# Performance work log

Hardware: AMD Instinct MI355X
Metric: run time of the kernel (lower is better)

Reference implementation:

```python
import jax, jax.numpy as jnp
import numpy as np

B, S, D = 2, 2048, 1024
H = 16  # num_content_vectors
HD = D // H


def setup_inputs() -> dict:
    key = jax.random.key(0)
    k1, k2, k3 = jax.random.split(key, 3)
    encoded = jax.random.normal(k1, (B, S, D), dtype=jnp.float32)
    # FusedDense(embed_dim, 2*embed_dim): weight [2D, D], bias [2D] (torch Linear layout)
    W = jax.random.normal(k2, (2 * D, D), dtype=jnp.float32) * (1.0 / np.sqrt(D))
    bias = jax.random.normal(k3, (2 * D,), dtype=jnp.float32) * 0.01
    return {"encoded": encoded, "W": W, "bias": bias}


def reference(encoded, W, bias):
    b, s, d = encoded.shape
    h = H
    hd = d // h
    # fused QK projection
    qk = jnp.einsum('bsd,ed->bse', encoded, W) + bias  # [b, s, 2d]
    qk = qk.reshape(b, s, 2, h, hd)
    q = qk[:, :, 0]  # [b, s, h, hd]
    k = qk[:, :, 1]
    scale = 1.0 / np.sqrt(hd)
    scores = jnp.einsum('bthd,bshd->bhts', q, k * scale)  # [b, h, s, s]
    causal_mask = jnp.triu(jnp.full((s, s), -10000.0, dtype=scores.dtype), 1)
    scores = scores + causal_mask
    return jax.nn.softmax(scores, axis=-1)
```

## Files before the change

### kernel.cpp

```cpp
#include <hip/hip_runtime.h>

#define S 2048
#define D 1024
#define H 16
#define HD 64

typedef _Float16 half8 __attribute__((ext_vector_type(8)));
typedef _Float16 half4v __attribute__((ext_vector_type(4)));
typedef float f32x4 __attribute__((ext_vector_type(4)));

__device__ __forceinline__ float fast_exp2(float x) {
#if __has_builtin(__builtin_amdgcn_exp2f)
    return __builtin_amdgcn_exp2f(x);
#else
    return exp2f(x);
#endif
}

__global__ __launch_bounds__(256) void cvt_f32_f16(const float* __restrict__ src,
                                                   _Float16* __restrict__ dst, int n4) {
    const int i = blockIdx.x * 256 + threadIdx.x;
    if (i >= n4) return;
    const float4 v = ((const float4*)src)[i];
    half4v h;
    h.x = (_Float16)v.x; h.y = (_Float16)v.y;
    h.z = (_Float16)v.z; h.w = (_Float16)v.w;
    ((half4v*)dst)[i] = h;
}

__global__ __launch_bounds__(256) void proj_mfma(const _Float16* __restrict__ Ah,
                                                 const _Float16* __restrict__ Wh,
                                                 const float* __restrict__ bias,
                                                 _Float16* __restrict__ qbuf,
                                                 _Float16* __restrict__ kbuf) {
    __shared__ __align__(16) _Float16 As[4][128][8];
    __shared__ __align__(16) _Float16 Bs[4][128][8];
    const int tid = threadIdx.x;
    const int w   = tid >> 6;
    const int l   = tid & 63;
    const int l15 = l & 15;
    const int l4  = l >> 4;
    const int wy  = w >> 1;
    const int wx  = w & 1;
    const int m0  = blockIdx.x * 128;
    const int n0  = blockIdx.y * 128;

    f32x4 acc[4][4] = {};

    for (int k0 = 0; k0 < D; k0 += 32) {
        if (k0) __syncthreads();
        #pragma unroll
        for (int p = 0; p < 2; ++p) {
            const int slot = p * 256 + tid;
            const int sub = slot >> 7, row = slot & 127;
            *(uint4*)&As[sub][row][0] = *(const uint4*)(Ah + (size_t)(m0 + row) * D + k0 + sub * 8);
            *(uint4*)&Bs[sub][row][0] = *(const uint4*)(Wh + (size_t)(n0 + row) * D + k0 + sub * 8);
        }
        __syncthreads();

        half8 af[4], bf[4];
        #pragma unroll
        for (int i = 0; i < 4; ++i)
            af[i] = *(const half8*)&As[l4][wy * 64 + i * 16 + l15][0];
        #pragma unroll
        for (int j = 0; j < 4; ++j)
            bf[j] = *(const half8*)&Bs[l4][wx * 64 + j * 16 + l15][0];
        #pragma unroll
        for (int i = 0; i < 4; ++i)
            #pragma unroll
            for (int j = 0; j < 4; ++j)
                acc[i][j] = __builtin_amdgcn_mfma_f32_16x16x32_f16(af[i], bf[j], acc[i][j], 0, 0, 0);
    }

    #pragma unroll
    for (int j = 0; j < 4; ++j) {
        const int e   = n0 + wx * 64 + j * 16 + l15;
        const bool isq = (e < D);
        const int eh  = isq ? e : (e - D);
        const int h   = eh >> 6;
        const int hd  = eh & 63;
        _Float16* dst = isq ? qbuf : kbuf;
        const float sc = isq ? 1.0f : 0.18033688f;
        const float bv = bias[e];
        #pragma unroll
        for (int i = 0; i < 4; ++i) {
            #pragma unroll
            for (int r = 0; r < 4; ++r) {
                const int m  = m0 + wy * 64 + i * 16 + l4 * 4 + r;
                const int bb = m >> 11;
                const int ss = m & (S - 1);
                dst[((size_t)(bb * H + h) * S + ss) * HD + hd] = (_Float16)((acc[i][j][r] + bv) * sc);
            }
        }
    }
}

__global__ __launch_bounds__(256) void attn_fused(const _Float16* __restrict__ qbuf,
                                                  const _Float16* __restrict__ kbuf,
                                                  float* __restrict__ out) {
    const int tid = threadIdx.x;
    const int w   = tid >> 6;
    const int l   = tid & 63;
    const int l15 = l & 15;
    const int l4  = l >> 4;

    const int bid  = blockIdx.x;
    const int xcd  = bid & 7;
    const int slot = bid >> 3;
    const int k    = slot >> 5;
    int tsr = slot & 31;
    if (k & 2) tsr = (tsr + 16) & 31;
    const int ts = (k & 1) ? (31 - tsr) : tsr;
    const int z  = xcd * 4 + k;
    const int t0 = ts * 64;

    const _Float16* Qg = qbuf + (size_t)z * S * HD;
    const _Float16* Kg = kbuf + (size_t)z * S * HD;
    float* outz = out + (size_t)z * S * S;

    const _Float16* qrow = Qg + (size_t)(t0 + w * 16 + l15) * HD + l4 * 8;
    const half8 qf0 = *(const half8*)qrow;
    const half8 qf1 = *(const half8*)(qrow + 32);

    const int nst  = ts + 1;
    const int trow = t0 + w * 16 + l4 * 4;
    const _Float16* kbase = Kg + (size_t)l15 * HD + l4 * 8;

    float sum_r[4] = {0.f, 0.f, 0.f, 0.f};

    for (int st = 0; st < nst; ++st) {
        const _Float16* kp = kbase + (size_t)st * (64 * HD);
        f32x4 c[4] = {};
        #pragma unroll
        for (int j = 0; j < 4; ++j) {
            const half8 kf0 = *(const half8*)(kp + j * (16 * HD));
            const half8 kf1 = *(const half8*)(kp + j * (16 * HD) + 32);
            c[j] = __builtin_amdgcn_mfma_f32_16x16x32_f16(qf0, kf0, c[j], 0, 0, 0);
            c[j] = __builtin_amdgcn_mfma_f32_16x16x32_f16(qf1, kf1, c[j], 0, 0, 0);
        }
        if (st == ts) {
            #pragma unroll
            for (int j = 0; j < 4; ++j) {
                const int scol = t0 + j * 16 + l15;
                #pragma unroll
                for (int r = 0; r < 4; ++r)
                    if (scol > trow + r) c[j][r] = -1e30f;
            }
        }
        #pragma unroll
        for (int j = 0; j < 4; ++j)
            #pragma unroll
            for (int r = 0; r < 4; ++r)
                sum_r[r] += fast_exp2(c[j][r]);
    }

    float inv_l[4];
    #pragma unroll
    for (int r = 0; r < 4; ++r) {
        float s = sum_r[r];
        s += __shfl_xor(s, 1, 16);
        s += __shfl_xor(s, 2, 16);
        s += __shfl_xor(s, 4, 16);
        s += __shfl_xor(s, 8, 16);
        inv_l[r] = 1.0f / s;
    }

    float* wrow = outz + (size_t)trow * S + l15;
    for (int st = 0; st < nst; ++st) {
        const int s0 = st * 64;
        const _Float16* kp = kbase + (size_t)st * (64 * HD);
        f32x4 c[4] = {};
        #pragma unroll
        for (int j = 0; j < 4; ++j) {
            const half8 kf0 = *(const half8*)(kp + j * (16 * HD));
            const half8 kf1 = *(const half8*)(kp + j * (16 * HD) + 32);
            c[j] = __builtin_amdgcn_mfma_f32_16x16x32_f16(qf0, kf0, c[j], 0, 0, 0);
            c[j] = __builtin_amdgcn_mfma_f32_16x16x32_f16(qf1, kf1, c[j], 0, 0, 0);
        }
        if (st == ts) {
            #pragma unroll
            for (int j = 0; j < 4; ++j) {
                const int scol = t0 + j * 16 + l15;
                #pragma unroll
                for (int r = 0; r < 4; ++r)
                    if (scol > trow + r) c[j][r] = -1e30f;
            }
        }
        #pragma unroll
        for (int r = 0; r < 4; ++r) {
            float* rowp = wrow + (size_t)r * S + s0;
            #pragma unroll
            for (int j = 0; j < 4; ++j)
                __builtin_nontemporal_store(fast_exp2(c[j][r]) * inv_l[r], rowp + j * 16);
        }
    }

    const int zc0 = t0 + 64;
    if (zc0 < S) {
        const int W4 = (S - zc0) >> 2;
        const f32x4 z4 = {0.f, 0.f, 0.f, 0.f};
        for (int row = w; row < 64; row += 4) {
            float* rp = outz + (size_t)(t0 + row) * S + zc0;
            for (int c4 = l; c4 < W4; c4 += 64)
                __builtin_nontemporal_store(z4, (f32x4*)(rp + c4 * 4));
        }
    }
}

extern "C" void kernel_launch(void* const* d_in, const int* in_sizes, int n_in,
                              void* d_out, int out_size, void* d_ws, size_t ws_size,
                              hipStream_t stream) {
    const float* enc  = (const float*)d_in[0];
    const float* Wf   = (const float*)d_in[1];
    const float* bias = (const float*)d_in[2];
    float* out = (float*)d_out;

    _Float16* enc_h = (_Float16*)d_ws;
    _Float16* w_h   = enc_h + (size_t)4096 * 1024;
    _Float16* qbuf  = w_h   + (size_t)2048 * 1024;
    _Float16* kbuf  = qbuf  + (size_t)32 * 2048 * 64;

    const int n4_enc = (4096 * 1024) / 4;
    const int n4_w   = (2048 * 1024) / 4;
    cvt_f32_f16<<<(n4_enc + 255) / 256, 256, 0, stream>>>(enc, enc_h, n4_enc);
    cvt_f32_f16<<<(n4_w   + 255) / 256, 256, 0, stream>>>(Wf, w_h, n4_w);

    proj_mfma<<<dim3(4096 / 128, 2048 / 128), 256, 0, stream>>>(enc_h, w_h, bias, qbuf, kbuf);

    attn_fused<<<dim3(1024), 256, 0, stream>>>(qbuf, kbuf, out);
}
```

Before: 653.6 us.

## Merge conversion kernels, use global_load_lds in projection, peel diagonal attention tile

Merges the two f32-to-f16 conversion launches into a single kernel. The projection GEMM now loads tiles straight from global memory into LDS with the global_load_lds builtin when the compiler provides it, skipping the trip through registers. In the attention kernel the diagonal causal tile is peeled out of both loops so the inner loops carry no masking branch, and launch bounds now request 4 blocks per CU. The work is dominated by writing the output, so these changes mainly trim launch overhead and per-iteration instruction count, and the occupancy hint may cause register spills.

New measurement: 635.3 us. 1.03x faster.

```diff
diff --git a/kernel.cpp b/kernel.cpp
--- a/kernel.cpp
+++ b/kernel.cpp
@@ -17,15 +17,34 @@
 #endif
 }
 
-__global__ __launch_bounds__(256) void cvt_f32_f16(const float* __restrict__ src,
-                                                   _Float16* __restrict__ dst, int n4) {
+#if __has_builtin(__builtin_amdgcn_global_load_lds)
+#define HAVE_GLDS 1
+#define GLDS16(gsrc, ldst)                                                     \
+    __builtin_amdgcn_global_load_lds(                                          \
+        (const __attribute__((address_space(1))) unsigned int*)(gsrc),         \
+        (__attribute__((address_space(3))) unsigned int*)(ldst), 16, 0, 0)
+#else
+#define HAVE_GLDS 0
+#endif
+
+#define N4_ENC (4096 * 1024 / 4)
+#define N4_W   (2048 * 1024 / 4)
+
+__global__ __launch_bounds__(256) void cvt_both(const float* __restrict__ enc,
+                                                const float* __restrict__ Wf,
+                                                _Float16* __restrict__ enc_h,
+                                                _Float16* __restrict__ w_h) {
     const int i = blockIdx.x * 256 + threadIdx.x;
-    if (i >= n4) return;
-    const float4 v = ((const float4*)src)[i];
+    const float* src;
+    _Float16* dst;
+    int j;
+    if (i < N4_ENC) { src = enc; dst = enc_h; j = i; }
+    else            { src = Wf;  dst = w_h;   j = i - N4_ENC; }
+    const float4 v = ((const float4*)src)[j];
     half4v h;
     h.x = (_Float16)v.x; h.y = (_Float16)v.y;
     h.z = (_Float16)v.z; h.w = (_Float16)v.w;
-    ((half4v*)dst)[i] = h;
+    ((half4v*)dst)[j] = h;
 }
 
 __global__ __launch_bounds__(256) void proj_mfma(const _Float16* __restrict__ Ah,
@@ -49,6 +68,16 @@
 
     for (int k0 = 0; k0 < D; k0 += 32) {
         if (k0) __syncthreads();
+#if HAVE_GLDS
+        {
+            const _Float16* a0 = Ah + (size_t)(m0 + l) * D + k0 + w * 8;
+            const _Float16* b0 = Wh + (size_t)(n0 + l) * D + k0 + w * 8;
+            GLDS16(a0,            &As[w][0][0]);
+            GLDS16(a0 + 64 * D,   &As[w][64][0]);
+            GLDS16(b0,            &Bs[w][0][0]);
+            GLDS16(b0 + 64 * D,   &Bs[w][64][0]);
+        }
+#else
         #pragma unroll
         for (int p = 0; p < 2; ++p) {
             const int slot = p * 256 + tid;
@@ -56,6 +85,7 @@
             *(uint4*)&As[sub][row][0] = *(const uint4*)(Ah + (size_t)(m0 + row) * D + k0 + sub * 8);
             *(uint4*)&Bs[sub][row][0] = *(const uint4*)(Wh + (size_t)(n0 + row) * D + k0 + sub * 8);
         }
+#endif
         __syncthreads();
 
         half8 af[4], bf[4];
@@ -95,9 +125,9 @@
     }
 }
 
-__global__ __launch_bounds__(256) void attn_fused(const _Float16* __restrict__ qbuf,
-                                                  const _Float16* __restrict__ kbuf,
-                                                  float* __restrict__ out) {
+__global__ __launch_bounds__(256, 4) void attn_fused(const _Float16* __restrict__ qbuf,
+                                                     const _Float16* __restrict__ kbuf,
+                                                     float* __restrict__ out) {
     const int tid = threadIdx.x;
     const int w   = tid >> 6;
     const int l   = tid & 63;
@@ -122,13 +152,12 @@
     const half8 qf0 = *(const half8*)qrow;
     const half8 qf1 = *(const half8*)(qrow + 32);
 
-    const int nst  = ts + 1;
     const int trow = t0 + w * 16 + l4 * 4;
     const _Float16* kbase = Kg + (size_t)l15 * HD + l4 * 8;
 
     float sum_r[4] = {0.f, 0.f, 0.f, 0.f};
 
-    for (int st = 0; st < nst; ++st) {
+    for (int st = 0; st < ts; ++st) {
         const _Float16* kp = kbase + (size_t)st * (64 * HD);
         f32x4 c[4] = {};
         #pragma unroll
@@ -137,21 +166,32 @@
             const half8 kf1 = *(const half8*)(kp + j * (16 * HD) + 32);
             c[j] = __builtin_amdgcn_mfma_f32_16x16x32_f16(qf0, kf0, c[j], 0, 0, 0);
             c[j] = __builtin_amdgcn_mfma_f32_16x16x32_f16(qf1, kf1, c[j], 0, 0, 0);
-        }
-        if (st == ts) {
-            #pragma unroll
-            for (int j = 0; j < 4; ++j) {
-                const int scol = t0 + j * 16 + l15;
-                #pragma unroll
-                for (int r = 0; r < 4; ++r)
-                    if (scol > trow + r) c[j][r] = -1e30f;
-            }
         }
         #pragma unroll
         for (int j = 0; j < 4; ++j)
             #pragma unroll
             for (int r = 0; r < 4; ++r)
                 sum_r[r] += fast_exp2(c[j][r]);
+    }
+    {
+        const _Float16* kp = kbase + (size_t)ts * (64 * HD);
+        f32x4 c[4] = {};
+        #pragma unroll
+        for (int j = 0; j < 4; ++j) {
+            const half8 kf0 = *(const half8*)(kp + j * (16 * HD));
+            const half8 kf1 = *(const half8*)(kp + j * (16 * HD) + 32);
+            c[j] = __builtin_amdgcn_mfma_f32_16x16x32_f16(qf0, kf0, c[j], 0, 0, 0);
+            c[j] = __builtin_amdgcn_mfma_f32_16x16x32_f16(qf1, kf1, c[j], 0, 0, 0);
+        }
+        #pragma unroll
+        for (int j = 0; j < 4; ++j) {
+            const int scol = t0 + j * 16 + l15;
+            #pragma unroll
+            for (int r = 0; r < 4; ++r) {
+                if (scol > trow + r) c[j][r] = -1e30f;
+                sum_r[r] += fast_exp2(c[j][r]);
+            }
+        }
     }
 
     float inv_l[4];
@@ -166,7 +206,7 @@
     }
 
     float* wrow = outz + (size_t)trow * S + l15;
-    for (int st = 0; st < nst; ++st) {
+    for (int st = 0; st < ts; ++st) {
         const int s0 = st * 64;
         const _Float16* kp = kbase + (size_t)st * (64 * HD);
         f32x4 c[4] = {};
@@ -177,14 +217,31 @@
             c[j] = __builtin_amdgcn_mfma_f32_16x16x32_f16(qf0, kf0, c[j], 0, 0, 0);
             c[j] = __builtin_amdgcn_mfma_f32_16x16x32_f16(qf1, kf1, c[j], 0, 0, 0);
         }
-        if (st == ts) {
-            #pragma unroll
-            for (int j = 0; j < 4; ++j) {
-                const int scol = t0 + j * 16 + l15;
-                #pragma unroll
-                for (int r = 0; r < 4; ++r)
-                    if (scol > trow + r) c[j][r] = -1e30f;
-            }
+        #pragma unroll
+        for (int r = 0; r < 4; ++r) {
+            float* rowp = wrow + (size_t)r * S + s0;
+            #pragma unroll
+            for (int j = 0; j < 4; ++j)
+                __builtin_nontemporal_store(fast_exp2(c[j][r]) * inv_l[r], rowp + j * 16);
+        }
+    }
+    {
+        const int s0 = ts * 64;
+        const _Float16* kp = kbase + (size_t)ts * (64 * HD);
+        f32x4 c[4] = {};
+        #pragma unroll
+        for (int j = 0; j < 4; ++j) {
+            const half8 kf0 = *(const half8*)(kp + j * (16 * HD));
+            const half8 kf1 = *(const half8*)(kp + j * (16 * HD) + 32);
+            c[j] = __builtin_amdgcn_mfma_f32_16x16x32_f16(qf0, kf0, c[j], 0, 0, 0);
+            c[j] = __builtin_amdgcn_mfma_f32_16x16x32_f16(qf1, kf1, c[j], 0, 0, 0);
+        }
+        #pragma unroll
+        for (int j = 0; j < 4; ++j) {
+            const int scol = t0 + j * 16 + l15;
+            #pragma unroll
+            for (int r = 0; r < 4; ++r)
+                if (scol > trow + r) c[j][r] = -1e30f;
         }
         #pragma unroll
         for (int r = 0; r < 4; ++r) {
@@ -220,10 +277,8 @@
     _Float16* qbuf  = w_h   + (size_t)2048 * 1024;
     _Float16* kbuf  = qbuf  + (size_t)32 * 2048 * 64;
 
-    const int n4_enc = (4096 * 1024) / 4;
-    const int n4_w   = (2048 * 1024) / 4;
-    cvt_f32_f16<<<(n4_enc + 255) / 256, 256, 0, stream>>>(enc, enc_h, n4_enc);
-    cvt_f32_f16<<<(n4_w   + 255) / 256, 256, 0, stream>>>(Wf, w_h, n4_w);
+    const int n4_total = N4_ENC + N4_W;
+    cvt_both<<<(n4_total + 255) / 256, 256, 0, stream>>>(enc, Wf, enc_h, w_h);
 
     proj_mfma<<<dim3(4096 / 128, 2048 / 128), 256, 0, stream>>>(enc_h, w_h, bias, qbuf, kbuf);
 
```
